# Kernel tuning notes

Hardware: AMD Instinct MI355X
Metric: run time of the kernel (lower is better)

The kernel has to match this reference:

```python
import jax, jax.numpy as jnp
import numpy as np
from jax import lax

B, L, D, H, OM = 16, 512, 2048, 512, 5


def _lstm(seq, wih, whh, bih, bhh):
    # seq: [T, B, F]; PyTorch gate order i, f, g, o
    Hh = whh.shape[1]
    Bb = seq.shape[1]
    def step(carry, xt):
        h, c = carry
        g = xt @ wih.T + h @ whh.T + bih + bhh
        i, f, gg, o = jnp.split(g, 4, axis=-1)
        c = jax.nn.sigmoid(f) * c + jax.nn.sigmoid(i) * jnp.tanh(gg)
        h = jax.nn.sigmoid(o) * jnp.tanh(c)
        return (h, c), h
    z = jnp.zeros((Bb, Hh), seq.dtype)
    _, hs = lax.scan(step, (z, z), seq)
    return hs  # [T, B, Hh]


def setup_inputs() -> dict:
    key = jax.random.key(0)
    ks = jax.random.split(key, 17)
    s = 0.02
    f32 = jnp.float32
    inp = {
        "x": jax.random.normal(ks[0], (B, L, D), f32),
        "wb": jax.random.normal(ks[1], (H, D, OM), f32) * s,
        "bb": jax.random.normal(ks[2], (H,), f32) * s,
        "wa": jax.random.normal(ks[3], (H, D, OM), f32) * s,
        "ba": jax.random.normal(ks[4], (H,), f32) * s,
        "wr": jax.random.normal(ks[5], (H, D, 2 * OM), f32) * s,
        "br": jax.random.normal(ks[6], (H,), f32) * s,
        "wih_f": jax.random.normal(ks[7], (4 * H, H + 1), f32) * s,
        "whh_f": jax.random.normal(ks[8], (4 * H, H), f32) * s,
        "bih_f": jax.random.normal(ks[9], (4 * H,), f32) * s,
        "bhh_f": jax.random.normal(ks[10], (4 * H,), f32) * s,
        "wih_r": jax.random.normal(ks[11], (4 * H, H + 1), f32) * s,
        "whh_r": jax.random.normal(ks[12], (4 * H, H), f32) * s,
        "bih_r": jax.random.normal(ks[13], (4 * H,), f32) * s,
        "bhh_r": jax.random.normal(ks[14], (4 * H,), f32) * s,
        "wfc": jax.random.normal(ks[15], (1, 2 * H), f32) * s,
        "bfc": jax.random.normal(ks[16], (1,), f32) * s,
    }
    return inp


def reference(x, wb, bb, wa, ba, wr, br, wih_f, whh_f, bih_f, bhh_f,
              wih_r, whh_r, bih_r, bhh_r, wfc, bfc):
    om = OM
    xc = jnp.transpose(x, (0, 2, 1))  # [B, D, L]
    conv = lambda w, b: lax.conv_general_dilated(
        xc, w, (1,), 'VALID', dimension_numbers=('NCH', 'OIH', 'NCH')) + b[None, :, None]
    cb = conv(wb, bb)  # [B, H, L-om+1]
    ca = conv(wa, ba)  # [B, H, L-om+1]
    cr = conv(wr, br)  # [B, H, L-2om+1]
    T = x.shape[1] - 2 * om  # number of centers c in [om, L-om)
    d_before = cb[:, :, 0:T]          # window [c-om, c) == conv output c-om
    d_after = ca[:, :, om:om + T]     # window [c, c+om) == conv output c
    vts_d = jnp.sum(d_before * d_after, axis=1, keepdims=True)  # [B, 1, T]
    vts_r = cr[:, :, 0:T]             # full window; pool over length-1 is identity
    vts_seq = jnp.concatenate([vts_r, vts_d], axis=1)  # [B, H+1, T]
    seq = jnp.transpose(vts_seq, (2, 0, 1))  # [T, B, H+1]
    hs_f = _lstm(seq, wih_f, whh_f, bih_f, bhh_f)
    hs_r = _lstm(seq[::-1], wih_r, whh_r, bih_r, bhh_r)[::-1]
    h = jnp.concatenate([hs_f, hs_r], axis=-1)  # [T, B, 2H]
    logits = jnp.einsum('tbh,h->tb', h, wfc[0]) + bfc[0]
    return jax.nn.sigmoid(jnp.transpose(logits))  # [B, T]
```

## Files before the change

### kernel.cpp

```cpp
#include <hip/hip_runtime.h>
#include <hip/hip_bf16.h>

typedef short v8s __attribute__((ext_vector_type(8)));
typedef float v4f __attribute__((ext_vector_type(4)));
typedef unsigned int u32;
typedef unsigned int u32x4 __attribute__((ext_vector_type(4)));
typedef unsigned short u16;
typedef unsigned long long u64;

__device__ __forceinline__ u16 f2bf(float f) {
    union { float f; u32 u; } x; x.f = f;
    u32 r = x.u + 0x7fffu + ((x.u >> 16) & 1u);
    return (u16)(r >> 16);
}
__device__ __forceinline__ float bf2f(u16 s) {
    union { u32 u; float f; } x; x.u = ((u32)s) << 16;
    return x.f;
}
__device__ __forceinline__ float sigmoidf_(float x) { return 1.f / (1.f + __expf(-x)); }
__device__ __forceinline__ float tanh_fast(float x) {
    float t = fminf(fmaxf(x, -15.f), 15.f);
    float e = __expf(2.f * t);
    return (e - 1.f) / (e + 1.f);
}

__global__ __launch_bounds__(256) void xbf_kernel(const float* __restrict__ x, u16* __restrict__ xbf, int n) {
    int i = (blockIdx.x * 256 + threadIdx.x) * 4;
    if (i + 3 < n) {
        float4 v = *(const float4*)(x + i);
        u16* d = xbf + i;
        d[0] = f2bf(v.x); d[1] = f2bf(v.y); d[2] = f2bf(v.z); d[3] = f2bf(v.w);
    }
}

__global__ __launch_bounds__(256) void packw_kernel(const float* __restrict__ wb, const float* __restrict__ wa,
                                                    const float* __restrict__ wr, u16* __restrict__ W1, u16* __restrict__ W2) {
    long e = ((long)blockIdx.x * 256 + threadIdx.x) * 4;
    int which = e >= (1024L * 10240) ? 1 : 0;
    long rem = e - (long)which * 1024 * 10240;
    int n = (int)(rem / 10240);
    int kap = (int)(rem % 10240);
    int tap = kap >> 11, d = kap & 2047;
    u16 o[4];
    if (n < 512) {
        const float* src = which ? wa : wb;
#pragma unroll
        for (int q = 0; q < 4; ++q) o[q] = f2bf(src[(long)n * 10240 + (d + q) * 5 + tap]);
    } else {
        const float* src = wr + (long)(n - 512) * 20480 + tap + (which ? 5 : 0);
#pragma unroll
        for (int q = 0; q < 4; ++q) o[q] = f2bf(src[(d + q) * 10]);
    }
    *(u64*)((which ? W2 : W1) + rem) = *(const u64*)o;
}

__global__ __launch_bounds__(256) void packwih_kernel(const float* __restrict__ wf, const float* __restrict__ wr,
                                                      u16* __restrict__ Bp) {
    int idx = blockIdx.x * 256 + threadIdx.x;
    int n = idx / 576, kap = idx % 576;
    int dir = n >> 11, g = n & 2047;
    const float* src = dir ? wr : wf;
    float v = (kap < 513) ? src[(long)g * 513 + kap] : 0.f;
    Bp[idx] = f2bf(v);
}

__global__ __launch_bounds__(256) void packwhh_kernel(const float* __restrict__ whf, const float* __restrict__ whr,
                                                      u16* __restrict__ W) {
    int idx = blockIdx.x * 256 + threadIdx.x;
    int dir = idx >> 20;
    float v = dir ? whr[idx & 1048575] : whf[idx];
    W[idx] = f2bf(v);
}

__global__ __launch_bounds__(256) void misc_kernel(const float* __restrict__ bihf, const float* __restrict__ bhhf,
                                                   const float* __restrict__ bihr, const float* __restrict__ bhhr,
                                                   float* __restrict__ bsum, u64* __restrict__ hbuf) {
    int i = blockIdx.x * 256 + threadIdx.x;
    if (i < 2048) bsum[i] = bihf[i] + bhhf[i];
    else if (i < 4096) bsum[i] = bihr[i - 2048] + bhhr[i - 2048];
    else if (i < 4096 + 16384) hbuf[i - 4096] = 0xFFFFFFFF00000000ULL;
}

__global__ __launch_bounds__(512, 1) void gemm_conv(const u16* __restrict__ A, const u16* __restrict__ B,
                                                    float* __restrict__ C, u32 row_base) {
    const int M = 8032, K = 10240, NT = 320;
    __shared__ char lds[98304];
    const int tn = blockIdx.x & 7;
    const int tm = blockIdx.x >> 3;
    const int tid = threadIdx.x, lane = tid & 63, w = tid >> 6;
    const int wm = w >> 1, wn = w & 1;
    const int lane15 = lane & 15, kgrp = lane >> 4;

    u32 asrc[2], bsrc;
#pragma unroll
    for (int r = 0; r < 2; ++r) {
        int l = r * 8192 + tid * 16;
        int rp = l >> 7, inner = l & 127;
        int innp = inner ^ ((rp & 7) << 4);
        int row = rp * 2 + (innp >> 6);
        int kb = innp & 63;
        int m = tm * 256 + row; if (m > M - 1) m = M - 1;
        asrc[r] = row_base + (u32)(m / 502) * (512u * 2048u) + (u32)(m % 502) * 2048u + (u32)(kb >> 1);
    }
    {
        int l = tid * 16;
        int rp = l >> 7, inner = l & 127;
        int innp = inner ^ ((rp & 7) << 4);
        int row = rp * 2 + (innp >> 6);
        int kb = innp & 63;
        bsrc = (u32)(tn * 128 + row) * (u32)K + (u32)(kb >> 1);
    }
    int aoff[4], boff[4];
#pragma unroll
    for (int i = 0; i < 4; ++i) {
        int row = wm * 64 + i * 16 + lane15;
        int rp = row >> 1;
        aoff[i] = rp * 128 + ((((row & 1) << 6) | (kgrp * 16)) ^ ((rp & 7) << 4));
        int rowb = wn * 64 + i * 16 + lane15;
        int rpb = rowb >> 1;
        boff[i] = rpb * 128 + ((((rowb & 1) << 6) | (kgrp * 16)) ^ ((rpb & 7) << 4));
    }

    v4f acc[4][4];
#pragma unroll
    for (int i = 0; i < 4; ++i)
#pragma unroll
        for (int j = 0; j < 4; ++j) acc[i][j] = (v4f){0.f, 0.f, 0.f, 0.f};

#define ISSUE(t) {                                                                          \
        int s_ = (t) & 3;                                                                   \
        __builtin_amdgcn_global_load_lds(                                                   \
            (const __attribute__((address_space(1))) u32*)(A + asrc[0] + (t) * 32),         \
            (__attribute__((address_space(3))) u32*)(lds + s_ * 16384 + w * 1024), 16, 0, 0);\
        __builtin_amdgcn_global_load_lds(                                                   \
            (const __attribute__((address_space(1))) u32*)(A + asrc[1] + (t) * 32),         \
            (__attribute__((address_space(3))) u32*)(lds + s_ * 16384 + 8192 + w * 1024), 16, 0, 0);\
        __builtin_amdgcn_global_load_lds(                                                   \
            (const __attribute__((address_space(1))) u32*)(B + bsrc + (t) * 32),            \
            (__attribute__((address_space(3))) u32*)(lds + 65536 + s_ * 8192 + w * 1024), 16, 0, 0);\
    }

    ISSUE(0) ISSUE(1) ISSUE(2)
    asm volatile("s_waitcnt vmcnt(6)" ::: "memory");
    __builtin_amdgcn_s_barrier();
    asm volatile("" ::: "memory");

    for (int kt = 0; kt < NT; ++kt) {
        const char* As = lds + (kt & 3) * 16384;
        const char* Bs = lds + 65536 + (kt & 3) * 8192;
        v8s a[4], b[4];
#pragma unroll
        for (int i = 0; i < 4; ++i) {
            a[i] = *(const v8s*)(As + aoff[i]);
            b[i] = *(const v8s*)(Bs + boff[i]);
        }
        if (kt + 3 < NT) ISSUE(kt + 3)
        __builtin_amdgcn_s_setprio(1);
#pragma unroll
        for (int i = 0; i < 4; ++i)
#pragma unroll
            for (int j = 0; j < 4; ++j)
                acc[i][j] = __builtin_amdgcn_mfma_f32_16x16x32_bf16(a[i], b[j], acc[i][j], 0, 0, 0);
        __builtin_amdgcn_s_setprio(0);
        if (kt + 3 < NT)      { asm volatile("s_waitcnt vmcnt(6)" ::: "memory"); }
        else if (kt + 2 < NT) { asm volatile("s_waitcnt vmcnt(3)" ::: "memory"); }
        else                  { asm volatile("s_waitcnt vmcnt(0)" ::: "memory"); }
        __builtin_amdgcn_s_barrier();
        asm volatile("" ::: "memory");
    }
#undef ISSUE

#pragma unroll
    for (int i = 0; i < 4; ++i)
#pragma unroll
        for (int j = 0; j < 4; ++j)
#pragma unroll
            for (int r = 0; r < 4; ++r) {
                int m = tm * 256 + wm * 64 + i * 16 + kgrp * 4 + r;
                int n = tn * 128 + wn * 64 + j * 16 + lane15;
                if (m < M) C[(long)m * 1024 + n] = acc[i][j][r];
            }
}

template <int OUTBF>
__global__ __launch_bounds__(256) void gemm_bf16(const u16* __restrict__ A, const u16* __restrict__ B,
                                                 void* __restrict__ Cv, int M, int N, int K, int ldc,
                                                 int row_div, u32 row_mul1, u32 row_mul2, u32 row_base) {
    __shared__ u16 ldsA[128 * 64];
    __shared__ u16 ldsB[128 * 64];
    const int ntn = N >> 7;
    const int nwg = gridDim.x;
    const int bid = blockIdx.x;
    const int swz = (bid & 7) * (nwg >> 3) + (bid >> 3);
    const int tm = swz / ntn, tn = swz % ntn;
    const int tid = threadIdx.x, lane = tid & 63, wv = tid >> 6;
    const int wm = wv >> 1, wn = wv & 1;
    const int qbase = wv * 4;

    u32 asrc[4], bsrc[4];
#pragma unroll
    for (int it = 0; it < 4; ++it) {
        int q = qbase + it;
        int r = q * 8 + (lane >> 3);
        int cb = ((lane & 7) * 16) ^ ((r & 7) << 4);
        int m = tm * 128 + r; if (m > M - 1) m = M - 1;
        asrc[it] = row_base + (u32)(m / row_div) * row_mul1 + (u32)(m % row_div) * row_mul2 + (u32)(cb >> 1);
        int n = tn * 128 + r;
        bsrc[it] = (u32)n * (u32)K + (u32)(cb >> 1);
    }

    v4f acc[4][4];
#pragma unroll
    for (int i = 0; i < 4; ++i)
#pragma unroll
        for (int j = 0; j < 4; ++j) acc[i][j] = (v4f){0.f, 0.f, 0.f, 0.f};

    const int KT = K >> 6;
    for (int kt = 0; kt < KT; ++kt) {
        const int k0 = kt << 6;
#pragma unroll
        for (int it = 0; it < 4; ++it) {
            int q = qbase + it;
            __builtin_amdgcn_global_load_lds(
                (const __attribute__((address_space(1))) u32*)(A + asrc[it] + k0),
                (__attribute__((address_space(3))) u32*)((char*)ldsA + q * 1024), 16, 0, 0);
            __builtin_amdgcn_global_load_lds(
                (const __attribute__((address_space(1))) u32*)(B + bsrc[it] + k0),
                (__attribute__((address_space(3))) u32*)((char*)ldsB + q * 1024), 16, 0, 0);
        }
        __syncthreads();
#pragma unroll
        for (int kk = 0; kk < 2; ++kk) {
            v8s af[4], bfr[4];
#pragma unroll
            for (int i = 0; i < 4; ++i) {
                int row = wm * 64 + i * 16 + (lane & 15);
                int cbyte = (kk * 64 + ((lane >> 4) * 16)) ^ ((row & 7) << 4);
                af[i] = *(const v8s*)((const char*)ldsA + row * 128 + cbyte);
                int rn = wn * 64 + i * 16 + (lane & 15);
                int cbn = (kk * 64 + ((lane >> 4) * 16)) ^ ((rn & 7) << 4);
                bfr[i] = *(const v8s*)((const char*)ldsB + rn * 128 + cbn);
            }
#pragma unroll
            for (int i = 0; i < 4; ++i)
#pragma unroll
                for (int j = 0; j < 4; ++j)
                    acc[i][j] = __builtin_amdgcn_mfma_f32_16x16x32_bf16(af[i], bfr[j], acc[i][j], 0, 0, 0);
        }
        __syncthreads();
    }
#pragma unroll
    for (int i = 0; i < 4; ++i)
#pragma unroll
        for (int j = 0; j < 4; ++j)
#pragma unroll
            for (int r = 0; r < 4; ++r) {
                int m = tm * 128 + wm * 64 + i * 16 + (lane >> 4) * 4 + r;
                int n = tn * 128 + wn * 64 + j * 16 + (lane & 15);
                if (m < M) {
                    if (OUTBF) ((u16*)Cv)[(long)m * ldc + n] = f2bf(acc[i][j][r]);
                    else       ((float*)Cv)[(long)m * ldc + n] = acc[i][j][r];
                }
            }
}

__global__ __launch_bounds__(256) void combine_kernel(const float* __restrict__ G1, const float* __restrict__ G2,
                                                      const float* __restrict__ bb, const float* __restrict__ ba,
                                                      const float* __restrict__ br, u16* __restrict__ seqpad) {
    int m = blockIdx.x;
    int b = m / 502, t = m % 502;
    int tid = threadIdx.x;
    const float* g1 = G1 + (long)m * 1024;
    const float* g2 = G2 + (long)m * 1024;
    u16* dst = seqpad + (long)(t * 16 + b) * 576;
    float part = 0.f;
#pragma unroll
    for (int rep = 0; rep < 2; ++rep) {
        int u = tid + rep * 256;
        float db = g1[u] + bb[u];
        float da = g2[u] + ba[u];
        part += db * da;
        float vr = g1[512 + u] + g2[512 + u] + br[u];
        dst[u] = f2bf(vr);
    }
#pragma unroll
    for (int off = 32; off; off >>= 1) part += __shfl_down(part, off, 64);
    __shared__ float red[4];
    if ((tid & 63) == 0) red[tid >> 6] = part;
    __syncthreads();
    if (tid == 0) dst[512] = f2bf(red[0] + red[1] + red[2] + red[3]);
    if (tid >= 1 && tid < 64) dst[512 + tid] = 0;
}

__global__ __launch_bounds__(256, 1) void lstm_kernel(const u16* __restrict__ P, const u16* __restrict__ whhbf,
                                                      const float* __restrict__ bsum, u64* hbuf,
                                                      u16* __restrict__ hs) {
    const int wg = blockIdx.x;
    const int dir = wg >> 4, j = wg & 15;
    const int tid = threadIdx.x, lane = tid & 63, w = tid >> 6;
    __shared__ u16 hls[16 * 512];
    __shared__ float gls[4][16][32];

    v8s bf[2][16];
    const u16* whd = whhbf + (long)dir * 2048 * 512;
#pragma unroll
    for (int nt = 0; nt < 2; ++nt) {
        int n = w * 512 + j * 32 + nt * 16 + (lane & 15);
#pragma unroll
        for (int kt = 0; kt < 16; ++kt)
            bf[nt][kt] = *(const v8s*)(whd + (long)n * 512 + kt * 32 + ((lane >> 4) * 8));
    }

    for (int i = tid; i < 8192; i += 256) hls[i] = 0;

    const int b_ = tid >> 4;
    const int u_ = (tid * 2) & 31;
    float c0 = 0.f, c1 = 0.f;
    u64* hb = hbuf + dir * 2 * 4096;
    const int col0 = w * 512 + j * 32 + (lane & 15);
    const float bs0 = bsum[dir * 2048 + col0];
    const float bs1 = bsum[dir * 2048 + col0 + 16];
    const u16* Pd = P + dir * 2048;

    float pv[2][4];
    {
        int tau = dir ? 501 : 0;
#pragma unroll
        for (int nt = 0; nt < 2; ++nt)
#pragma unroll
            for (int r = 0; r < 4; ++r)
                pv[nt][r] = bf2f(Pd[(long)(tau * 16 + ((lane >> 4) * 4 + r)) * 4096 + col0 + nt * 16]);
    }
    __syncthreads();

    for (int s = 0; s < 502; ++s) {
        const int tau = dir ? (501 - s) : s;
        if (s > 0) {
            const u64* slotp = hb + ((s - 1) & 1) * 4096;
            const u32 want = (u32)(s - 1);
            u64 base = (u64)slotp + (u64)tid * 16;
            u64 a0 = base,          a1 = base + 4096,  a2 = base + 8192,  a3 = base + 12288;
            u64 a4 = base + 16384,  a5 = base + 20480, a6 = base + 24576, a7 = base + 28672;
            u32x4 w0, w1, w2, w3, w4, w5, w6, w7;
            for (;;) {
                asm volatile(
                    "global_load_dwordx4 %[w0], %[a0], off sc1\n\t"
                    "global_load_dwordx4 %[w1], %[a1], off sc1\n\t"
                    "global_load_dwordx4 %[w2], %[a2], off sc1\n\t"
                    "global_load_dwordx4 %[w3], %[a3], off sc1\n\t"
                    "global_load_dwordx4 %[w4], %[a4], off sc1\n\t"
                    "global_load_dwordx4 %[w5], %[a5], off sc1\n\t"
                    "global_load_dwordx4 %[w6], %[a6], off sc1\n\t"
                    "global_load_dwordx4 %[w7], %[a7], off sc1\n\t"
                    "s_waitcnt vmcnt(0)"
                    : [w0]"=v"(w0), [w1]"=v"(w1), [w2]"=v"(w2), [w3]"=v"(w3),
                      [w4]"=v"(w4), [w5]"=v"(w5), [w6]"=v"(w6), [w7]"=v"(w7)
                    : [a0]"v"(a0), [a1]"v"(a1), [a2]"v"(a2), [a3]"v"(a3),
                      [a4]"v"(a4), [a5]"v"(a5), [a6]"v"(a6), [a7]"v"(a7)
                    : "memory");
                u32 ok = (w0[1] == want) + (w0[3] == want) + (w1[1] == want) + (w1[3] == want)
                       + (w2[1] == want) + (w2[3] == want) + (w3[1] == want) + (w3[3] == want)
                       + (w4[1] == want) + (w4[3] == want) + (w5[1] == want) + (w5[3] == want)
                       + (w6[1] == want) + (w6[3] == want) + (w7[1] == want) + (w7[3] == want);
                if (ok == 16) break;
            }
#define FILL(rep, pay0, pay1) {                                                             \
            int i0 = tid * 2 + (rep) * 512;                                                 \
            int bb2 = i0 >> 8; int p = i0 & 255;                                            \
            int bo = (bb2 << 10) + ((p << 2) ^ ((bb2 & 7) << 4));                           \
            *(u32*)((char*)hls + bo) = (pay0);                                              \
            int p1 = p + 1;                                                                 \
            int bo1 = (bb2 << 10) + ((p1 << 2) ^ ((bb2 & 7) << 4));                         \
            *(u32*)((char*)hls + bo1) = (pay1); }
            FILL(0, w0[0], w0[2]) FILL(1, w1[0], w1[2]) FILL(2, w2[0], w2[2]) FILL(3, w3[0], w3[2])
            FILL(4, w4[0], w4[2]) FILL(5, w5[0], w5[2]) FILL(6, w6[0], w6[2]) FILL(7, w7[0], w7[2])
#undef FILL
        }
        __syncthreads();
        v4f a0a, a1a, a0b = (v4f){0, 0, 0, 0}, a1b = (v4f){0, 0, 0, 0};
#pragma unroll
        for (int r = 0; r < 4; ++r) { a0a[r] = pv[0][r] + bs0; a1a[r] = pv[1][r] + bs1; }
#pragma unroll
        for (int kt = 0; kt < 16; kt += 2) {
            int row = lane & 15;
            int cb0 = (kt * 64 + ((lane >> 4) * 16)) ^ ((row & 7) << 4);
            int cb1 = ((kt + 1) * 64 + ((lane >> 4) * 16)) ^ ((row & 7) << 4);
            v8s af0 = *(const v8s*)((const char*)hls + row * 1024 + cb0);
            v8s af1 = *(const v8s*)((const char*)hls + row * 1024 + cb1);
            a0a = __builtin_amdgcn_mfma_f32_16x16x32_bf16(af0, bf[0][kt], a0a, 0, 0, 0);
            a1a = __builtin_amdgcn_mfma_f32_16x16x32_bf16(af0, bf[1][kt], a1a, 0, 0, 0);
            a0b = __builtin_amdgcn_mfma_f32_16x16x32_bf16(af1, bf[0][kt + 1], a0b, 0, 0, 0);
            a1b = __builtin_amdgcn_mfma_f32_16x16x32_bf16(af1, bf[1][kt + 1], a1b, 0, 0, 0);
        }
#pragma unroll
        for (int r = 0; r < 4; ++r) {
            gls[w][(lane >> 4) * 4 + r][(lane & 15)] = a0a[r] + a0b[r];
            gls[w][(lane >> 4) * 4 + r][16 + (lane & 15)] = a1a[r] + a1b[r];
        }
        __syncthreads();
        float i0 = gls[0][b_][u_],     f0 = gls[1][b_][u_],     g0 = gls[2][b_][u_],     o0 = gls[3][b_][u_];
        float i1 = gls[0][b_][u_ + 1], f1 = gls[1][b_][u_ + 1], g1v = gls[2][b_][u_ + 1], o1 = gls[3][b_][u_ + 1];
        c0 = sigmoidf_(f0) * c0 + sigmoidf_(i0) * tanh_fast(g0);
        c1 = sigmoidf_(f1) * c1 + sigmoidf_(i1) * tanh_fast(g1v);
        float h0 = sigmoidf_(o0) * tanh_fast(c0);
        float h1 = sigmoidf_(o1) * tanh_fast(c1);
        u32 hw = (u32)f2bf(h0) | ((u32)f2bf(h1) << 16);
        int gi = (b_ * 512 + j * 32 + u_) >> 1;
        __hip_atomic_store(hb + (s & 1) * 4096 + gi, (u64)hw | ((u64)(u32)s << 32),
                           __ATOMIC_RELAXED, __HIP_MEMORY_SCOPE_AGENT);
        *(u32*)(hs + (((long)(dir * 502 + tau) * 16 + b_) * 512 + j * 32 + u_)) = hw;
        if (s + 1 < 502) {
            int tau2 = dir ? (500 - s) : (s + 1);
#pragma unroll
            for (int nt = 0; nt < 2; ++nt)
#pragma unroll
                for (int r = 0; r < 4; ++r)
                    pv[nt][r] = bf2f(Pd[(long)(tau2 * 16 + ((lane >> 4) * 4 + r)) * 4096 + col0 + nt * 16]);
        }
    }
}

__global__ __launch_bounds__(256) void final_kernel(const u16* __restrict__ hs, const float* __restrict__ wfc,
                                                    const float* __restrict__ bfc, float* __restrict__ out) {
    int m = blockIdx.x;
    int t = m >> 4, b = m & 15;
    int tid = threadIdx.x;
    const u16* hf = hs + ((long)t * 16 + b) * 512;
    const u16* hr = hs + ((long)(502 + t) * 16 + b) * 512;
    float part = 0.f;
#pragma unroll
    for (int rep = 0; rep < 2; ++rep) {
        int u = tid + rep * 256;
        part += bf2f(hf[u]) * wfc[u] + bf2f(hr[u]) * wfc[512 + u];
    }
#pragma unroll
    for (int off = 32; off; off >>= 1) part += __shfl_down(part, off, 64);
    __shared__ float red[4];
    if ((tid & 63) == 0) red[tid >> 6] = part;
    __syncthreads();
    if (tid == 0) {
        float lg = red[0] + red[1] + red[2] + red[3] + bfc[0];
        out[(long)b * 502 + t] = 1.f / (1.f + __expf(-lg));
    }
}

extern "C" void kernel_launch(void* const* d_in, const int* in_sizes, int n_in,
                              void* d_out, int out_size, void* d_ws, size_t ws_size,
                              hipStream_t stream) {
    const float* x     = (const float*)d_in[0];
    const float* wb    = (const float*)d_in[1];
    const float* bb    = (const float*)d_in[2];
    const float* wa    = (const float*)d_in[3];
    const float* ba    = (const float*)d_in[4];
    const float* wr    = (const float*)d_in[5];
    const float* br    = (const float*)d_in[6];
    const float* wih_f = (const float*)d_in[7];
    const float* whh_f = (const float*)d_in[8];
    const float* bih_f = (const float*)d_in[9];
    const float* bhh_f = (const float*)d_in[10];
    const float* wih_r = (const float*)d_in[11];
    const float* whh_r = (const float*)d_in[12];
    const float* bih_r = (const float*)d_in[13];
    const float* bhh_r = (const float*)d_in[14];
    const float* wfc   = (const float*)d_in[15];
    const float* bfc   = (const float*)d_in[16];
    float* out = (float*)d_out;

    char* ws = (char*)d_ws;
    u16* xbf = (u16*)ws;
    u16* W1  = (u16*)(ws + 33554432);
    u16* W2  = (u16*)(ws + 54525952);
    u16* Pb  = (u16*)ws;
    char* r2 = ws + 75497472;
    float* G1 = (float*)r2;
    float* G2 = (float*)(r2 + 32899072);
    u16*  hs  = (u16*)r2;
    char* r3 = r2 + 65798144;
    u16*  seqp = (u16*)r3;
    u16*  wihp = (u16*)(r3 + 9252864);
    u16*  whhb = (u16*)(r3 + 13971456);
    float* bsum= (float*)(r3 + 18165760);
    u64*  hbuf = (u64*)(r3 + 18182144);

    xbf_kernel<<<16384, 256, 0, stream>>>(x, xbf, 16 * 512 * 2048);
    packw_kernel<<<20480, 256, 0, stream>>>(wb, wa, wr, W1, W2);
    packwih_kernel<<<9216, 256, 0, stream>>>(wih_f, wih_r, wihp);
    packwhh_kernel<<<8192, 256, 0, stream>>>(whh_f, whh_r, whhb);
    misc_kernel<<<80, 256, 0, stream>>>(bih_f, bhh_f, bih_r, bhh_r, bsum, hbuf);

    gemm_conv<<<256, 512, 0, stream>>>(xbf, W1, G1, 0u);
    gemm_conv<<<256, 512, 0, stream>>>(xbf, W2, G2, 5u * 2048u);
    combine_kernel<<<8032, 256, 0, stream>>>(G1, G2, bb, ba, br, seqp);
    gemm_bf16<1><<<63 * 32, 256, 0, stream>>>(seqp, wihp, Pb, 8032, 4096, 576, 4096,
                                              8032, 0u, 576u, 0u);
    lstm_kernel<<<32, 256, 0, stream>>>(Pb, whhb, bsum, hbuf, hs);
    final_kernel<<<8032, 256, 0, stream>>>(hs, wfc, bfc, out);
}
```

Before: 1.677 ms.

## Replace input-projection GEMM with 256x128 tiles and 4-stage async LDS pipeline

Replaces the generic bf16 GEMM used for the LSTM input projection with a specialized kernel. It uses 256x128 tiles over 512 threads and a 4-slot LDS ring buffer, keeping three k-tiles of global-to-LDS loads in flight. Waits use fine-grained vmcnt with one barrier per k-step, and MFMA runs at raised wave priority. The aim is to hide global-load latency and reduce barrier stalls, at the cost of 96KB LDS and one workgroup per CU.

```diff
diff --git a/kernel.cpp b/kernel.cpp
--- a/kernel.cpp
+++ b/kernel.cpp
@@ -182,31 +182,45 @@
             }
 }
 
-template <int OUTBF>
-__global__ __launch_bounds__(256) void gemm_bf16(const u16* __restrict__ A, const u16* __restrict__ B,
-                                                 void* __restrict__ Cv, int M, int N, int K, int ldc,
-                                                 int row_div, u32 row_mul1, u32 row_mul2, u32 row_base) {
-    __shared__ u16 ldsA[128 * 64];
-    __shared__ u16 ldsB[128 * 64];
-    const int ntn = N >> 7;
-    const int nwg = gridDim.x;
+__global__ __launch_bounds__(512, 1) void gemm_proj(const u16* __restrict__ A, const u16* __restrict__ B,
+                                                    u16* __restrict__ C) {
+    const int M = 8032, K = 576, NT = 18;
+    __shared__ char lds[98304];
     const int bid = blockIdx.x;
-    const int swz = (bid & 7) * (nwg >> 3) + (bid >> 3);
-    const int tm = swz / ntn, tn = swz % ntn;
-    const int tid = threadIdx.x, lane = tid & 63, wv = tid >> 6;
-    const int wm = wv >> 1, wn = wv & 1;
-    const int qbase = wv * 4;
-
-    u32 asrc[4], bsrc[4];
-#pragma unroll
-    for (int it = 0; it < 4; ++it) {
-        int q = qbase + it;
-        int r = q * 8 + (lane >> 3);
-        int cb = ((lane & 7) * 16) ^ ((r & 7) << 4);
-        int m = tm * 128 + r; if (m > M - 1) m = M - 1;
-        asrc[it] = row_base + (u32)(m / row_div) * row_mul1 + (u32)(m % row_div) * row_mul2 + (u32)(cb >> 1);
-        int n = tn * 128 + r;
-        bsrc[it] = (u32)n * (u32)K + (u32)(cb >> 1);
+    const int swz = (bid & 7) * 128 + (bid >> 3);
+    const int tm = swz >> 5, tn = swz & 31;
+    const int tid = threadIdx.x, lane = tid & 63, w = tid >> 6;
+    const int wm = w >> 1, wn = w & 1;
+    const int lane15 = lane & 15, kgrp = lane >> 4;
+
+    u32 asrc[2], bsrc;
+#pragma unroll
+    for (int r = 0; r < 2; ++r) {
+        int l = r * 8192 + tid * 16;
+        int rp = l >> 7, inner = l & 127;
+        int innp = inner ^ ((rp & 7) << 4);
+        int row = rp * 2 + (innp >> 6);
+        int kb = innp & 63;
+        int m = tm * 256 + row; if (m > M - 1) m = M - 1;
+        asrc[r] = (u32)m * (u32)K + (u32)(kb >> 1);
+    }
+    {
+        int l = tid * 16;
+        int rp = l >> 7, inner = l & 127;
+        int innp = inner ^ ((rp & 7) << 4);
+        int row = rp * 2 + (innp >> 6);
+        int kb = innp & 63;
+        bsrc = (u32)(tn * 128 + row) * (u32)K + (u32)(kb >> 1);
+    }
+    int aoff[4], boff[4];
+#pragma unroll
+    for (int i = 0; i < 4; ++i) {
+        int row = wm * 64 + i * 16 + lane15;
+        int rp = row >> 1;
+        aoff[i] = rp * 128 + ((((row & 1) << 6) | (kgrp * 16)) ^ ((rp & 7) << 4));
+        int rowb = wn * 64 + i * 16 + lane15;
+        int rpb = rowb >> 1;
+        boff[i] = rpb * 128 + ((((rowb & 1) << 6) | (kgrp * 16)) ^ ((rpb & 7) << 4));
     }
 
     v4f acc[4][4];
@@ -215,52 +229,58 @@
 #pragma unroll
         for (int j = 0; j < 4; ++j) acc[i][j] = (v4f){0.f, 0.f, 0.f, 0.f};
 
-    const int KT = K >> 6;
-    for (int kt = 0; kt < KT; ++kt) {
-        const int k0 = kt << 6;
-#pragma unroll
-        for (int it = 0; it < 4; ++it) {
-            int q = qbase + it;
-            __builtin_amdgcn_global_load_lds(
-                (const __attribute__((address_space(1))) u32*)(A + asrc[it] + k0),
-                (__attribute__((address_space(3))) u32*)((char*)ldsA + q * 1024), 16, 0, 0);
-            __builtin_amdgcn_global_load_lds(
-                (const __attribute__((address_space(1))) u32*)(B + bsrc[it] + k0),
-                (__attribute__((address_space(3))) u32*)((char*)ldsB + q * 1024), 16, 0, 0);
+#define ISSUE(t) {                                                                          \
+        int s_ = (t) & 3;                                                                   \
+        __builtin_amdgcn_global_load_lds(                                                   \
+            (const __attribute__((address_space(1))) u32*)(A + asrc[0] + (t) * 32),         \
+            (__attribute__((address_space(3))) u32*)(lds + s_ * 16384 + w * 1024), 16, 0, 0);\
+        __builtin_amdgcn_global_load_lds(                                                   \
+            (const __attribute__((address_space(1))) u32*)(A + asrc[1] + (t) * 32),         \
+            (__attribute__((address_space(3))) u32*)(lds + s_ * 16384 + 8192 + w * 1024), 16, 0, 0);\
+        __builtin_amdgcn_global_load_lds(                                                   \
+            (const __attribute__((address_space(1))) u32*)(B + bsrc + (t) * 32),            \
+            (__attribute__((address_space(3))) u32*)(lds + 65536 + s_ * 8192 + w * 1024), 16, 0, 0);\
+    }
+
+    ISSUE(0) ISSUE(1) ISSUE(2)
+    asm volatile("s_waitcnt vmcnt(6)" ::: "memory");
+    __builtin_amdgcn_s_barrier();
+    asm volatile("" ::: "memory");
+
+    for (int kt = 0; kt < NT; ++kt) {
+        const char* As = lds + (kt & 3) * 16384;
+        const char* Bs = lds + 65536 + (kt & 3) * 8192;
+        v8s a[4], b[4];
+#pragma unroll
+        for (int i = 0; i < 4; ++i) {
+            a[i] = *(const v8s*)(As + aoff[i]);
+            b[i] = *(const v8s*)(Bs + boff[i]);
         }
-        __syncthreads();
-#pragma unroll
-        for (int kk = 0; kk < 2; ++kk) {
-            v8s af[4], bfr[4];
-#pragma unroll
-            for (int i = 0; i < 4; ++i) {
-                int row = wm * 64 + i * 16 + (lane & 15);
-                int cbyte = (kk * 64 + ((lane >> 4) * 16)) ^ ((row & 7) << 4);
-                af[i] = *(const v8s*)((const char*)ldsA + row * 128 + cbyte);
-                int rn = wn * 64 + i * 16 + (lane & 15);
-                int cbn = (kk * 64 + ((lane >> 4) * 16)) ^ ((rn & 7) << 4);
-                bfr[i] = *(const v8s*)((const char*)ldsB + rn * 128 + cbn);
-            }
-#pragma unroll
-            for (int i = 0; i < 4; ++i)
-#pragma unroll
-                for (int j = 0; j < 4; ++j)
-                    acc[i][j] = __builtin_amdgcn_mfma_f32_16x16x32_bf16(af[i], bfr[j], acc[i][j], 0, 0, 0);
-        }
-        __syncthreads();
-    }
+        if (kt + 3 < NT) ISSUE(kt + 3)
+        __builtin_amdgcn_s_setprio(1);
+#pragma unroll
+        for (int i = 0; i < 4; ++i)
+#pragma unroll
+            for (int j = 0; j < 4; ++j)
+                acc[i][j] = __builtin_amdgcn_mfma_f32_16x16x32_bf16(a[i], b[j], acc[i][j], 0, 0, 0);
+        __builtin_amdgcn_s_setprio(0);
+        if (kt + 3 < NT)      { asm volatile("s_waitcnt vmcnt(6)" ::: "memory"); }
+        else if (kt + 2 < NT) { asm volatile("s_waitcnt vmcnt(3)" ::: "memory"); }
+        else                  { asm volatile("s_waitcnt vmcnt(0)" ::: "memory"); }
+        __builtin_amdgcn_s_barrier();
+        asm volatile("" ::: "memory");
+    }
+#undef ISSUE
+
 #pragma unroll
     for (int i = 0; i < 4; ++i)
 #pragma unroll
         for (int j = 0; j < 4; ++j)
 #pragma unroll
             for (int r = 0; r < 4; ++r) {
-                int m = tm * 128 + wm * 64 + i * 16 + (lane >> 4) * 4 + r;
-                int n = tn * 128 + wn * 64 + j * 16 + (lane & 15);
-                if (m < M) {
-                    if (OUTBF) ((u16*)Cv)[(long)m * ldc + n] = f2bf(acc[i][j][r]);
-                    else       ((float*)Cv)[(long)m * ldc + n] = acc[i][j][r];
-                }
+                int m = tm * 256 + wm * 64 + i * 16 + kgrp * 4 + r;
+                int n = tn * 128 + wn * 64 + j * 16 + lane15;
+                if (m < M) C[(long)m * 4096 + n] = f2bf(acc[i][j][r]);
             }
 }
 
@@ -491,8 +511,7 @@
     gemm_conv<<<256, 512, 0, stream>>>(xbf, W1, G1, 0u);
     gemm_conv<<<256, 512, 0, stream>>>(xbf, W2, G2, 5u * 2048u);
     combine_kernel<<<8032, 256, 0, stream>>>(G1, G2, bb, ba, br, seqp);
-    gemm_bf16<1><<<63 * 32, 256, 0, stream>>>(seqp, wihp, Pb, 8032, 4096, 576, 4096,
-                                              8032, 0u, 576u, 0u);
+    gemm_proj<<<1024, 512, 0, stream>>>(seqp, wihp, Pb);
     lstm_kernel<<<32, 256, 0, stream>>>(Pb, whhb, bsum, hbuf, hs);
     final_kernel<<<8032, 256, 0, stream>>>(hs, wfc, bfc, out);
 }
```

Result: no change. 1.685 ms (+0.5%).
